# Kernel optimization log

Hardware: AMD Instinct MI355X
Metric: run time of the kernel (lower is better)

The kernel has to match this reference:

```python
import jax, jax.numpy as jnp
import numpy as np
import math

N, S, E, BS = 8, 8192, 256, 8


def setup_inputs() -> dict:
    key = jax.random.key(0)
    k1, k2, k3 = jax.random.split(key, 3)
    seq_vector = jax.random.normal(k1, (N, S, E), dtype=jnp.float32)
    # Conv1d weight [target_dim, source_dim] (kernel size 1 squeezed), default torch init scale
    bound = 1.0 / math.sqrt(E)
    W = jax.random.uniform(k2, (E, E), minval=-bound, maxval=bound, dtype=jnp.float32)
    sigma = math.sqrt(1.0 / (BS * E))
    bias = jax.random.uniform(k3, (BS,), minval=-sigma, maxval=sigma, dtype=jnp.float32)
    return {"seq_vector": seq_vector, "W": W, "bias": bias}


def reference(seq_vector, W, bias):
    n, s, e = seq_vector.shape
    bs = bias.shape[0]
    # 1x1 conv == per-token projection: [N,S,E] x [T,E] -> [N,S,T]
    features = jnp.einsum('nse,te->nst', seq_vector, W)
    # group sequence into blocks: [N, S//bs, bs, T]
    fb = features.reshape(n, s // bs, bs, -1)
    # blockwise causal (strictly lower-triangular) sum == exclusive cumsum over block dim
    excl = jnp.cumsum(fb, axis=2) - fb
    # position i gets bias[i]; position 0 additionally gets bias[0] a second time
    b_eff = bias.at[0].add(bias[0])  # [bs]
    out = excl + b_eff[None, None, :, None]
    return out.reshape(n, s, -1)
```

## Files before the change

kernel.cpp:

```cpp
#include <hip/hip_runtime.h>


typedef short short8 __attribute__((ext_vector_type(8)));
typedef float floatx4 __attribute__((ext_vector_type(4)));
typedef unsigned short ushort4v __attribute__((ext_vector_type(4)));

typedef const __attribute__((address_space(1))) unsigned int* gas_u32p;
typedef __attribute__((address_space(3))) unsigned int* las_u32p;

#define WAIT_VMCNT(n) __builtin_amdgcn_s_waitcnt(0x0F70 | ((n) & 0xF) | ((((n) >> 4) & 0x3) << 14))

__device__ __forceinline__ void gl2lds16(const float* g, float* l) {
    __builtin_amdgcn_global_load_lds((gas_u32p)(const void*)g, (las_u32p)(void*)l, 16, 0, 0);
}

__device__ __forceinline__ unsigned short f2bf(float f) {
    union { float f; unsigned int u; } v;
    v.f = f;
    unsigned int u = v.u + 0x7fffu + ((v.u >> 16) & 1u);
    return (unsigned short)(u >> 16);
}

__device__ __forceinline__ short8 pack8(float4 f0, float4 f1) {
    short8 r;
    r[0] = (short)f2bf(f0.x); r[1] = (short)f2bf(f0.y);
    r[2] = (short)f2bf(f0.z); r[3] = (short)f2bf(f0.w);
    r[4] = (short)f2bf(f1.x); r[5] = (short)f2bf(f1.y);
    r[6] = (short)f2bf(f1.z); r[7] = (short)f2bf(f1.w);
    return r;
}

__global__ __launch_bounds__(256) void wconv_kernel(
    const float* __restrict__ W, unsigned short* __restrict__ Wb)
{
    const int i = (blockIdx.x * 256 + threadIdx.x) * 4;
    float4 f = *(const float4*)(W + i);
    ushort4v v;
    v[0] = f2bf(f.x); v[1] = f2bf(f.y); v[2] = f2bf(f.z); v[3] = f2bf(f.w);
    *(ushort4v*)(Wb + i) = v;
}

__global__ __launch_bounds__(256) void bcl_gemm_kernel(
    const float* __restrict__ X, const unsigned short* __restrict__ Wb,
    const float* __restrict__ bias, float* __restrict__ out)
{
    __shared__ float buf[3][128 * 32];

    const int tid  = threadIdx.x;
    const int lane = tid & 63;
    const int w    = tid >> 6;
    const int bx   = blockIdx.x;
    const int mg   = bx >> 1;
    const int ng   = bx & 1;

    const int cl = lane & 15;
    const int q  = lane >> 4;

    const int srow = lane >> 3;
    const int sseg = (lane & 7) ^ srow;
    const float* gsrc0 = X + (size_t)(mg * 128 + w * 32 + srow) * 256 + sseg * 4;

#define STAGE(c, b)                                                            \
    do {                                                                       \
        const float* _g = gsrc0 + (c) * 32;                                    \
        _Pragma("unroll")                                                      \
        for (int _j = 0; _j < 4; ++_j)                                         \
            gl2lds16(_g + _j * 8 * 256, &buf[b][(w * 32 + _j * 8) * 32]);      \
    } while (0)

    const unsigned short* bBase = Wb + (size_t)(ng * 128 + cl) * 256 + q * 8;

    floatx4 acc[2][8];
    #pragma unroll
    for (int mt = 0; mt < 2; ++mt)
        #pragma unroll
        for (int nt = 0; nt < 8; ++nt)
            acc[mt][nt] = (floatx4){0.f, 0.f, 0.f, 0.f};

    STAGE(0, 0);
    STAGE(1, 1);

    #pragma unroll
    for (int c = 0; c < 8; ++c) {
        WAIT_VMCNT(4);
        __builtin_amdgcn_sched_barrier(0);

        short8 Bf[8];
        #pragma unroll
        for (int nt = 0; nt < 8; ++nt)
            Bf[nt] = *(const short8*)(bBase + nt * 16 * 256 + c * 32);

        float4 af[2][2];
        #pragma unroll
        for (int mt = 0; mt < 2; ++mt)
            #pragma unroll
            for (int h = 0; h < 2; ++h)
                af[mt][h] = *(const float4*)
                    &buf[c % 3][(w * 32 + mt * 16 + cl) * 32 +
                                ((((q << 1) | h) ^ (cl & 7)) << 2)];

        if (c + 2 < 8) STAGE(c + 2, (c + 2) % 3);

        short8 a[2];
        a[0] = pack8(af[0][0], af[0][1]);
        a[1] = pack8(af[1][0], af[1][1]);

        #pragma unroll
        for (int mt = 0; mt < 2; ++mt)
            #pragma unroll
            for (int nt = 0; nt < 8; ++nt)
                acc[mt][nt] = __builtin_amdgcn_mfma_f32_16x16x32_bf16(
                    a[mt], Bf[nt], acc[mt][nt], 0, 0, 0);
    }

    float be[4];
    {
        const int off = (q & 1) * 4;
        be[0] = bias[off + 0];
        be[1] = bias[off + 1];
        be[2] = bias[off + 2];
        be[3] = bias[off + 3];
        if (off == 0) be[0] += bias[0];
    }

    float* epi = &buf[0][w * 32 * 32];

    #pragma unroll
    for (int p = 0; p < 4; ++p) {
        const int mt = p >> 1;
        const bool act = ((q >> 1) == (p & 1));
        #pragma unroll
        for (int nt = 0; nt < 8; ++nt) {
            floatx4 v = acc[mt][nt];
            float p1 = v[0];
            float p2 = p1 + v[1];
            float p3 = p2 + v[2];
            float tot = p3 + v[3];
            float below = __shfl_up(tot, 16);
            float p0 = 0.f;
            if (q & 1) { p0 = below; p1 += below; p2 += below; p3 += below; }
            if (act) {
                float* dst = epi + (q & 1) * 4 * 128 + nt * 16 + cl;
                dst[0]   = p0 + be[0];
                dst[128] = p1 + be[1];
                dst[256] = p2 + be[2];
                dst[384] = p3 + be[3];
            }
        }
        #pragma unroll
        for (int k = 0; k < 4; ++k) {
            const int r   = k * 2 + (lane >> 5);
            const int c32 = lane & 31;
            floatx4 vv = *(const floatx4*)&epi[r * 128 + c32 * 4];
            const size_t grow = (size_t)(mg * 128 + w * 32 + p * 8 + r);
            *(floatx4*)&out[grow * 256 + ng * 128 + c32 * 4] = vv;
        }
    }
#undef STAGE
}

extern "C" void kernel_launch(void* const* d_in, const int* in_sizes, int n_in,
                              void* d_out, int out_size, void* d_ws, size_t ws_size,
                              hipStream_t stream)
{
    const float* X = (const float*)d_in[0];
    const float* W = (const float*)d_in[1];
    const float* B = (const float*)d_in[2];
    float* out = (float*)d_out;
    unsigned short* Wb = (unsigned short*)d_ws;

    wconv_kernel<<<dim3(64), dim3(256), 0, stream>>>(W, Wb);
    bcl_gemm_kernel<<<dim3(1024), dim3(256), 0, stream>>>(X, Wb, B, out);
}
```

Before: 144.1 us.

## Split output columns into quarters, keep W in registers, deepen LDS pipeline

Each block now computes a 128x64 output tile instead of 128x128, with a grouped block-index mapping so the four column blocks sharing an X tile run close together. The block's bf16 W slice is preloaded once into registers, removing per-chunk W loads. The LDS ring grows from 3 to 4 buffers with prefetch distance 3, and packing uses hardware bf16 conversion. In exchange, X tiles are read by twice as many blocks, and register and LDS use per block rise.

Measured after the change: 154.4 us. 7.1% more time.

```diff
diff --git a/kernel.cpp b/kernel.cpp
--- a/kernel.cpp
+++ b/kernel.cpp
@@ -1,4 +1,5 @@
 #include <hip/hip_runtime.h>
+#include <hip/hip_bf16.h>
 
 
 typedef short short8 __attribute__((ext_vector_type(8)));
@@ -22,12 +23,14 @@
 }
 
 __device__ __forceinline__ short8 pack8(float4 f0, float4 f1) {
-    short8 r;
-    r[0] = (short)f2bf(f0.x); r[1] = (short)f2bf(f0.y);
-    r[2] = (short)f2bf(f0.z); r[3] = (short)f2bf(f0.w);
-    r[4] = (short)f2bf(f1.x); r[5] = (short)f2bf(f1.y);
-    r[6] = (short)f2bf(f1.z); r[7] = (short)f2bf(f1.w);
-    return r;
+    union { __hip_bfloat162 h; unsigned int u; } c0, c1, c2, c3;
+    c0.h = __float22bfloat162_rn({f0.x, f0.y});
+    c1.h = __float22bfloat162_rn({f0.z, f0.w});
+    c2.h = __float22bfloat162_rn({f1.x, f1.y});
+    c3.h = __float22bfloat162_rn({f1.z, f1.w});
+    union { short8 s; unsigned int u[4]; } r;
+    r.u[0] = c0.u; r.u[1] = c1.u; r.u[2] = c2.u; r.u[3] = c3.u;
+    return r.s;
 }
 
 __global__ __launch_bounds__(256) void wconv_kernel(
@@ -44,51 +47,58 @@
     const float* __restrict__ X, const unsigned short* __restrict__ Wb,
     const float* __restrict__ bias, float* __restrict__ out)
 {
-    __shared__ float buf[3][128 * 32];
+    __shared__ float buf[4][128 * 32];
 
     const int tid  = threadIdx.x;
     const int lane = tid & 63;
     const int w    = tid >> 6;
     const int bx   = blockIdx.x;
-    const int mg   = bx >> 1;
-    const int ng   = bx & 1;
+    const int mg   = ((bx >> 5) << 3) | (bx & 7);
+    const int ng   = (bx >> 3) & 3;
 
     const int cl = lane & 15;
     const int q  = lane >> 4;
+
+    short8 Brg[4][8];
+    {
+        const unsigned short* bBase = Wb + (size_t)(ng * 64 + cl) * 256 + q * 8;
+        #pragma unroll
+        for (int nt = 0; nt < 4; ++nt)
+            #pragma unroll
+            for (int c = 0; c < 8; ++c)
+                Brg[nt][c] = *(const short8*)(bBase + nt * 16 * 256 + c * 32);
+    }
 
     const int srow = lane >> 3;
     const int sseg = (lane & 7) ^ srow;
     const float* gsrc0 = X + (size_t)(mg * 128 + w * 32 + srow) * 256 + sseg * 4;
 
-#define STAGE(c, b)                                                            \
+#define STAGE(c)                                                               \
     do {                                                                       \
         const float* _g = gsrc0 + (c) * 32;                                    \
+        float* _l = &buf[(c) & 3][w * 32 * 32];                                \
         _Pragma("unroll")                                                      \
         for (int _j = 0; _j < 4; ++_j)                                         \
-            gl2lds16(_g + _j * 8 * 256, &buf[b][(w * 32 + _j * 8) * 32]);      \
+            gl2lds16(_g + _j * 8 * 256, _l + _j * 8 * 32);                     \
     } while (0)
 
-    const unsigned short* bBase = Wb + (size_t)(ng * 128 + cl) * 256 + q * 8;
-
-    floatx4 acc[2][8];
+    floatx4 acc[2][4];
     #pragma unroll
     for (int mt = 0; mt < 2; ++mt)
         #pragma unroll
-        for (int nt = 0; nt < 8; ++nt)
+        for (int nt = 0; nt < 4; ++nt)
             acc[mt][nt] = (floatx4){0.f, 0.f, 0.f, 0.f};
 
-    STAGE(0, 0);
-    STAGE(1, 1);
+    STAGE(0);
+    STAGE(1);
+    STAGE(2);
 
     #pragma unroll
     for (int c = 0; c < 8; ++c) {
-        WAIT_VMCNT(4);
+        if (c < 6)       WAIT_VMCNT(8);
+        else if (c == 6) WAIT_VMCNT(4);
+        else             WAIT_VMCNT(0);
         __builtin_amdgcn_sched_barrier(0);
-
-        short8 Bf[8];
-        #pragma unroll
-        for (int nt = 0; nt < 8; ++nt)
-            Bf[nt] = *(const short8*)(bBase + nt * 16 * 256 + c * 32);
 
         float4 af[2][2];
         #pragma unroll
@@ -96,22 +106,23 @@
             #pragma unroll
             for (int h = 0; h < 2; ++h)
                 af[mt][h] = *(const float4*)
-                    &buf[c % 3][(w * 32 + mt * 16 + cl) * 32 +
+                    &buf[c & 3][(w * 32 + mt * 16 + cl) * 32 +
                                 ((((q << 1) | h) ^ (cl & 7)) << 2)];
 
-        if (c + 2 < 8) STAGE(c + 2, (c + 2) % 3);
+        if (c + 3 < 8) STAGE(c + 3);
 
-        short8 a[2];
-        a[0] = pack8(af[0][0], af[0][1]);
-        a[1] = pack8(af[1][0], af[1][1]);
+        short8 a0 = pack8(af[0][0], af[0][1]);
+        short8 a1 = pack8(af[1][0], af[1][1]);
 
         #pragma unroll
-        for (int mt = 0; mt < 2; ++mt)
-            #pragma unroll
-            for (int nt = 0; nt < 8; ++nt)
-                acc[mt][nt] = __builtin_amdgcn_mfma_f32_16x16x32_bf16(
-                    a[mt], Bf[nt], acc[mt][nt], 0, 0, 0);
+        for (int nt = 0; nt < 4; ++nt) {
+            acc[0][nt] = __builtin_amdgcn_mfma_f32_16x16x32_bf16(
+                a0, Brg[nt][c], acc[0][nt], 0, 0, 0);
+            acc[1][nt] = __builtin_amdgcn_mfma_f32_16x16x32_bf16(
+                a1, Brg[nt][c], acc[1][nt], 0, 0, 0);
+        }
     }
+#undef STAGE
 
     float be[4];
     {
@@ -127,10 +138,10 @@
 
     #pragma unroll
     for (int p = 0; p < 4; ++p) {
-        const int mt = p >> 1;
+        const int mt  = p >> 1;
         const bool act = ((q >> 1) == (p & 1));
         #pragma unroll
-        for (int nt = 0; nt < 8; ++nt) {
+        for (int nt = 0; nt < 4; ++nt) {
             floatx4 v = acc[mt][nt];
             float p1 = v[0];
             float p2 = p1 + v[1];
@@ -140,23 +151,22 @@
             float p0 = 0.f;
             if (q & 1) { p0 = below; p1 += below; p2 += below; p3 += below; }
             if (act) {
-                float* dst = epi + (q & 1) * 4 * 128 + nt * 16 + cl;
+                float* dst = epi + (q & 1) * 4 * 64 + nt * 16 + cl;
                 dst[0]   = p0 + be[0];
-                dst[128] = p1 + be[1];
-                dst[256] = p2 + be[2];
-                dst[384] = p3 + be[3];
+                dst[64]  = p1 + be[1];
+                dst[128] = p2 + be[2];
+                dst[192] = p3 + be[3];
             }
         }
         #pragma unroll
-        for (int k = 0; k < 4; ++k) {
-            const int r   = k * 2 + (lane >> 5);
-            const int c32 = lane & 31;
-            floatx4 vv = *(const floatx4*)&epi[r * 128 + c32 * 4];
+        for (int k = 0; k < 2; ++k) {
+            const int r   = k * 4 + (lane >> 4);
+            const int c16 = lane & 15;
+            floatx4 vv = *(const floatx4*)&epi[r * 64 + c16 * 4];
             const size_t grow = (size_t)(mg * 128 + w * 32 + p * 8 + r);
-            *(floatx4*)&out[grow * 256 + ng * 128 + c32 * 4] = vv;
+            *(floatx4*)&out[grow * 256 + ng * 64 + c16 * 4] = vv;
         }
     }
-#undef STAGE
 }
 
 extern "C" void kernel_launch(void* const* d_in, const int* in_sizes, int n_in,
@@ -170,5 +180,5 @@
     unsigned short* Wb = (unsigned short*)d_ws;
 
     wconv_kernel<<<dim3(64), dim3(256), 0, stream>>>(W, Wb);
-    bcl_gemm_kernel<<<dim3(1024), dim3(256), 0, stream>>>(X, Wb, B, out);
+    bcl_gemm_kernel<<<dim3(2048), dim3(256), 0, stream>>>(X, Wb, B, out);
 }
```
